# Kernel tuning notes

Measured on AMD Instinct MI355X. Metric: run time of the kernel, lower is better.

## Reference

```python
import jax, jax.numpy as jnp
import numpy as np

N_NODES = 100_000
N_EDGES = 1_000_000
LATENT = 64
HID_ATOM = 256
HID_BOND = 256
RBF_DIM = 32
RBF_DMAX = 10.0
N_ATOM_TYPES = 10
N_CHARGES = 6
N_BOND_ORDERS = 5


def setup_inputs() -> dict:
    key = jax.random.key(0)
    ks = jax.random.split(key, 12)
    positions = jax.random.normal(ks[0], (N_NODES, 3), dtype=jnp.float32) * 5.0
    quantized = jax.random.normal(ks[1], (N_NODES, LATENT), dtype=jnp.float32)
    pair_indices = jax.random.randint(ks[2], (N_EDGES, 2), 0, N_NODES, dtype=jnp.int64)
    s = 0.05
    return {
        "positions": positions,
        "quantized": quantized,
        "pair_indices": pair_indices,
        "aW1": jax.random.normal(ks[3], (LATENT, HID_ATOM), jnp.float32) * s,
        "ab1": jnp.zeros((HID_ATOM,), jnp.float32),
        "aW2": jax.random.normal(ks[4], (HID_ATOM, N_ATOM_TYPES + N_CHARGES), jnp.float32) * s,
        "ab2": jnp.zeros((N_ATOM_TYPES + N_CHARGES,), jnp.float32),
        "bW1": jax.random.normal(ks[5], (LATENT + RBF_DIM, HID_BOND), jnp.float32) * s,
        "bb1": jnp.zeros((HID_BOND,), jnp.float32),
        "bW2": jax.random.normal(ks[6], (HID_BOND, N_BOND_ORDERS), jnp.float32) * s,
        "bb2": jnp.zeros((N_BOND_ORDERS,), jnp.float32),
    }


def _norm_no_nan(x, eps=1e-8):
    # L2 norm over last axis, clamped to avoid NaN gradients at 0
    return jnp.sqrt(jnp.maximum(jnp.sum(x * x, axis=-1), eps))


def _rbf(D, D_min=0.0, D_max=RBF_DMAX, D_count=RBF_DIM):
    mu = jnp.linspace(D_min, D_max, D_count, dtype=D.dtype)  # [D_count]
    sigma = (D_max - D_min) / D_count
    z = (D[..., None] - mu) / sigma
    return jnp.exp(-z * z)  # [E, D_count]


def reference(positions, quantized, pair_indices, aW1, ab1, aW2, ab2, bW1, bb1, bW2, bb2):
    src = pair_indices[:, 0]
    dst = pair_indices[:, 1]
    # pairwise distances -> RBF expansion
    x_i = positions[src]            # [E, 3]
    x_j = positions[dst]
    dists = _rbf(_norm_no_nan(x_i - x_j))  # [E, rbf_dim]
    # atom decoder (per node)
    h = jax.nn.relu(quantized @ aW1 + ab1)
    scalar_logits = h @ aW2 + ab2
    atom_type_logits = scalar_logits[:, :N_ATOM_TYPES]
    atom_charge_logits = scalar_logits[:, N_ATOM_TYPES:]
    # bond decoder (per edge): gathered latent sum concat RBF
    pair_feats = quantized[src] + quantized[dst]           # [E, latent]
    combined = jnp.concatenate([pair_feats, dists], axis=1)  # [E, latent+rbf]
    hb = jax.nn.relu(combined @ bW1 + bb1)
    bond_order_logits = hb @ bW2 + bb2
    return (atom_type_logits, atom_charge_logits, bond_order_logits)
```

## Files before the change

kernel.cpp:

```cpp
#include <hip/hip_runtime.h>
#include <hip/hip_bf16.h>

typedef __bf16 bf16x8 __attribute__((ext_vector_type(8)));
typedef __bf16 bf16x4 __attribute__((ext_vector_type(4)));
typedef float  f32x4  __attribute__((ext_vector_type(4)));

#define N_NODES 100000
#define N_EDGES 1000000
#define LATENT  64
#define HID     256
#define RBF_DIM 32
#define NTYPES  10
#define NCHG    6
#define NBOND   5

#define ATOM_TILES (N_NODES / 32)
#define ANBLK 512

#define ETILE  32
#define ETILES (N_EDGES / ETILE)
#define ENBLK  768

struct __align__(16) ASmem {
    __bf16 qs[32][72];
    __bf16 hsE[32][264];
    float  red[4][2][4][64];
};

template<bool EMIT_QB>
__global__ __launch_bounds__(256, 2) void atom_kernel(
    const float* __restrict__ q,   const float* __restrict__ aW1,
    const float* __restrict__ ab1, const float* __restrict__ aW2,
    const float* __restrict__ ab2, float* __restrict__ outA,
    float* __restrict__ outB,      __bf16* __restrict__ qb)
{
    __shared__ ASmem sm;
    const int t    = threadIdx.x;
    const int w    = t >> 6;
    const int lane = t & 63;
    const int l15  = lane & 15;
    const int hi   = lane >> 4;
    const int wcol = w * 64;

    bf16x8 aw1f[2][4];
    #pragma unroll
    for (int kb = 0; kb < 2; ++kb)
        #pragma unroll
        for (int nt = 0; nt < 4; ++nt) {
            const int nn = wcol + nt * 16 + l15;
            const int k0 = kb * 32 + hi * 8;
            bf16x8 v;
            #pragma unroll
            for (int j = 0; j < 8; ++j) v[j] = (__bf16)aW1[(k0 + j) * HID + nn];
            aw1f[kb][nt] = v;
        }
    bf16x8 aw2f[2];
    #pragma unroll
    for (int kk = 0; kk < 2; ++kk) {
        const int k0 = (w * 2 + kk) * 32 + hi * 8;
        bf16x8 v;
        #pragma unroll
        for (int j = 0; j < 8; ++j) v[j] = (__bf16)aW2[(k0 + j) * 16 + l15];
        aw2f[kk] = v;
    }
    float4 b1v[4];
    #pragma unroll
    for (int nt = 0; nt < 4; ++nt)
        b1v[nt] = *(const float4*)(&ab1[wcol + nt * 16 + hi * 4]);

    const int m_st = t >> 3;
    const int p_st = t & 7;

    for (int tile = blockIdx.x; tile < ATOM_TILES; tile += ANBLK) {
        const int node0 = tile * 32;
        {
            const float* qr = q + (size_t)(node0 + m_st) * 64 + p_st * 8;
            const float4 a0 = *(const float4*)(qr);
            const float4 a1 = *(const float4*)(qr + 4);
            bf16x8 v;
            v[0] = (__bf16)a0.x; v[1] = (__bf16)a0.y; v[2] = (__bf16)a0.z; v[3] = (__bf16)a0.w;
            v[4] = (__bf16)a1.x; v[5] = (__bf16)a1.y; v[6] = (__bf16)a1.z; v[7] = (__bf16)a1.w;
            *(bf16x8*)(&sm.qs[m_st][p_st * 8]) = v;
            if constexpr (EMIT_QB)
                *(bf16x8*)(qb + (size_t)(node0 + m_st) * 64 + p_st * 8) = v;
        }
        __syncthreads();

        f32x4 acc[2][4];
        #pragma unroll
        for (int mt = 0; mt < 2; ++mt)
            #pragma unroll
            for (int nt = 0; nt < 4; ++nt)
                #pragma unroll
                for (int r = 0; r < 4; ++r)
                    acc[mt][nt][r] = ((const float*)&b1v[nt])[r];

        #pragma unroll
        for (int kb = 0; kb < 2; ++kb)
            #pragma unroll
            for (int mt = 0; mt < 2; ++mt) {
                const bf16x8 bq = *(const bf16x8*)((const char*)&sm.qs[0][0]
                                   + (mt * 16 + l15) * 144 + kb * 64 + hi * 16);
                #pragma unroll
                for (int nt = 0; nt < 4; ++nt)
                    acc[mt][nt] = __builtin_amdgcn_mfma_f32_16x16x32_bf16(
                        aw1f[kb][nt], bq, acc[mt][nt], 0, 0, 0);
            }

        #pragma unroll
        for (int mt = 0; mt < 2; ++mt)
            #pragma unroll
            for (int nt = 0; nt < 4; ++nt) {
                bf16x4 hv;
                #pragma unroll
                for (int r = 0; r < 4; ++r)
                    hv[r] = (__bf16)fmaxf(acc[mt][nt][r], 0.f);
                *(bf16x4*)(&sm.hsE[mt * 16 + l15][wcol + nt * 16 + hi * 4]) = hv;
            }
        __syncthreads();

        f32x4 acc2[2];
        {
            f32x4 z = {0.f, 0.f, 0.f, 0.f};
            acc2[0] = z; acc2[1] = z;
        }
        #pragma unroll
        for (int mt = 0; mt < 2; ++mt)
            #pragma unroll
            for (int kk = 0; kk < 2; ++kk) {
                const int kb = w * 2 + kk;
                const bf16x8 af = *(const bf16x8*)((const char*)&sm.hsE[0][0]
                                   + (mt * 16 + l15) * 528 + kb * 64 + hi * 16);
                acc2[mt] = __builtin_amdgcn_mfma_f32_16x16x32_bf16(
                    af, aw2f[kk], acc2[mt], 0, 0, 0);
            }
        #pragma unroll
        for (int mt = 0; mt < 2; ++mt)
            #pragma unroll
            for (int r = 0; r < 4; ++r)
                sm.red[w][mt][r][lane] = acc2[mt][r];
        __syncthreads();

        {
            const int o  = t & 15;
            const int m0 = t >> 4;
            #pragma unroll
            for (int half = 0; half < 2; ++half) {
                const int m  = m0 + half * 16;
                const int mt = m >> 4, rr = m & 15;
                const int hh = rr >> 2, r = rr & 3;
                float s = ab2[o];
                #pragma unroll
                for (int ww = 0; ww < 4; ++ww) s += sm.red[ww][mt][r][hh * 16 + o];
                const int node = node0 + m;
                if (o < NTYPES) outA[node * NTYPES + o] = s;
                else            outB[node * NCHG + (o - NTYPES)] = s;
            }
        }
        __syncthreads();
    }
}

struct __align__(16) ESmem {
    __bf16 comb[2][ETILE][104];
    __bf16 hsE[ETILE][264];
    float  red[2][4][2][4][64];
};

__device__ __forceinline__ void bar_lgkm() {
    asm volatile("s_waitcnt lgkmcnt(0)" ::: "memory");
    __builtin_amdgcn_s_barrier();
}

template<bool USEBF>
__global__ __launch_bounds__(256, 3) void edge_kernel(
    const float* __restrict__ pos, const float* __restrict__ qf,
    const __bf16* __restrict__ qb, const int* __restrict__ pair,
    const float* __restrict__ bW1, const float* __restrict__ bb1,
    const float* __restrict__ bW2, const float* __restrict__ bb2,
    float* __restrict__ outC)
{
    __shared__ ESmem sm;
    const int t    = threadIdx.x;
    const int w    = t >> 6;
    const int lane = t & 63;
    const int l15  = lane & 15;
    const int hi   = lane >> 4;
    const int hid0 = w * 64;

    bf16x8 bw1f[3][4];
    #pragma unroll
    for (int kb = 0; kb < 3; ++kb)
        #pragma unroll
        for (int nt = 0; nt < 4; ++nt) {
            const int nn = hid0 + nt * 16 + l15;
            const int k0 = kb * 32 + hi * 8;
            bf16x8 v;
            #pragma unroll
            for (int j = 0; j < 8; ++j) v[j] = (__bf16)bW1[(k0 + j) * HID + nn];
            bw1f[kb][nt] = v;
        }
    bf16x8 w2f[2];
    #pragma unroll
    for (int kk = 0; kk < 2; ++kk) {
        const int k0 = hid0 + kk * 32 + hi * 8;
        bf16x8 v;
        #pragma unroll
        for (int j = 0; j < 8; ++j)
            v[j] = (l15 < NBOND) ? (__bf16)bW2[(k0 + j) * NBOND + l15] : (__bf16)0.f;
        w2f[kk] = v;
    }
    float4 b1v[4];
    #pragma unroll
    for (int nt = 0; nt < 4; ++nt)
        b1v[nt] = *(const float4*)(&bb1[hid0 + nt * 16 + hi * 4]);

    const int e_loc = t >> 3;
    const int p     = t & 7;

    int tile = blockIdx.x;
    bf16x8 gs, gd;
    float4 fs0, fs1, fd0, fd1;
    float  ps0, ps1, ps2, pd0, pd1, pd2;
    int2 pA = ((const int2*)pair)[(size_t)tile * ETILE + e_loc];
    #define GATHER(pN)                                                            \
        if constexpr (USEBF) {                                                    \
            gs = *(const bf16x8*)(qb + ((unsigned)(pN).x * 64u + (unsigned)(p*8)));\
            gd = *(const bf16x8*)(qb + ((unsigned)(pN).y * 64u + (unsigned)(p*8)));\
        } else {                                                                  \
            fs0 = *(const float4*)(qf + ((unsigned)(pN).x * 64u + (unsigned)(p*8)));     \
            fs1 = *(const float4*)(qf + ((unsigned)(pN).x * 64u + (unsigned)(p*8) + 4u));\
            fd0 = *(const float4*)(qf + ((unsigned)(pN).y * 64u + (unsigned)(p*8)));     \
            fd1 = *(const float4*)(qf + ((unsigned)(pN).y * 64u + (unsigned)(p*8) + 4u));\
        }                                                                         \
        ps0 = pos[(unsigned)(pN).x * 3u];  ps1 = pos[(unsigned)(pN).x * 3u + 1u]; \
        ps2 = pos[(unsigned)(pN).x * 3u + 2u];                                    \
        pd0 = pos[(unsigned)(pN).y * 3u];  pd1 = pos[(unsigned)(pN).y * 3u + 1u]; \
        pd2 = pos[(unsigned)(pN).y * 3u + 2u];

    #define STAGE(buf)                                                            \
        {                                                                         \
            bf16x8 cv;                                                            \
            if constexpr (USEBF) {                                                \
                _Pragma("unroll")                                                 \
                for (int j = 0; j < 8; ++j)                                       \
                    cv[j] = (__bf16)((float)gs[j] + (float)gd[j]);                \
            } else {                                                              \
                cv[0] = (__bf16)(fs0.x + fd0.x); cv[1] = (__bf16)(fs0.y + fd0.y); \
                cv[2] = (__bf16)(fs0.z + fd0.z); cv[3] = (__bf16)(fs0.w + fd0.w); \
                cv[4] = (__bf16)(fs1.x + fd1.x); cv[5] = (__bf16)(fs1.y + fd1.y); \
                cv[6] = (__bf16)(fs1.z + fd1.z); cv[7] = (__bf16)(fs1.w + fd1.w); \
            }                                                                     \
            *(bf16x8*)(&sm.comb[buf][e_loc][p * 8]) = cv;                         \
            const float dx = ps0 - pd0, dy = ps1 - pd1, dz = ps2 - pd2;           \
            const float D  = sqrtf(fmaxf(dx * dx + dy * dy + dz * dz, 1e-8f));    \
            bf16x4 rv;                                                            \
            _Pragma("unroll")                                                     \
            for (int j = 0; j < 4; ++j) {                                         \
                const float mu = (float)(p * 4 + j) * (10.0f / 31.0f);            \
                const float z  = (D - mu) * 3.2f;                                 \
                rv[j] = (__bf16)__expf(-z * z);                                   \
            }                                                                     \
            *(bf16x4*)(&sm.comb[buf][e_loc][64 + p * 4]) = rv;                    \
        }

    GATHER(pA);
    {
        const int tn = tile + ENBLK;
        pA = ((const int2*)pair)[(tn < ETILES ? (size_t)tn * ETILE : 0) + e_loc];
    }
    STAGE(0);
    GATHER(pA);
    {
        const int tn = tile + 2 * ENBLK;
        pA = ((const int2*)pair)[(tn < ETILES ? (size_t)tn * ETILE : 0) + e_loc];
    }
    bar_lgkm();

    int cur = 0;
    int e0_prev = -1;

    for (; tile < ETILES; tile += ENBLK) {
        const int e0 = tile * ETILE;

        if (e0_prev >= 0 && t < 160) {
            const int m = t / 5, o = t % 5;
            const int mt = m >> 4, rr = m & 15;
            const int hh = rr >> 2, r = rr & 3;
            float s = bb2[o];
            #pragma unroll
            for (int ww = 0; ww < 4; ++ww)
                s += sm.red[cur ^ 1][ww][mt][r][hh * 16 + o];
            outC[(size_t)(e0_prev + m) * NBOND + o] = s;
        }

        STAGE(cur ^ 1);

        GATHER(pA);
        {
            const int tn = tile + 3 * ENBLK;
            pA = ((const int2*)pair)[(tn < ETILES ? (size_t)tn * ETILE : 0) + e_loc];
        }

        f32x4 acc[2][4];
        #pragma unroll
        for (int mt = 0; mt < 2; ++mt)
            #pragma unroll
            for (int nt = 0; nt < 4; ++nt)
                #pragma unroll
                for (int r = 0; r < 4; ++r)
                    acc[mt][nt][r] = ((const float*)&b1v[nt])[r];

        #pragma unroll
        for (int kb = 0; kb < 3; ++kb)
            #pragma unroll
            for (int mt = 0; mt < 2; ++mt) {
                const bf16x8 bf = *(const bf16x8*)((const char*)&sm.comb[cur][0][0]
                                   + (mt * 16 + l15) * 208 + kb * 64 + hi * 16);
                #pragma unroll
                for (int nt = 0; nt < 4; ++nt)
                    acc[mt][nt] = __builtin_amdgcn_mfma_f32_16x16x32_bf16(
                        bw1f[kb][nt], bf, acc[mt][nt], 0, 0, 0);
            }
        #pragma unroll
        for (int mt = 0; mt < 2; ++mt)
            #pragma unroll
            for (int nt = 0; nt < 4; ++nt) {
                bf16x4 hv;
                #pragma unroll
                for (int r = 0; r < 4; ++r)
                    hv[r] = (__bf16)fmaxf(acc[mt][nt][r], 0.f);
                *(bf16x4*)((char*)&sm.hsE[0][0]
                           + (mt * 16 + l15) * 528 + (hid0 + nt * 16 + hi * 4) * 2) = hv;
            }

        {
            f32x4 acc2[2];
            {
                f32x4 z = {0.f, 0.f, 0.f, 0.f};
                acc2[0] = z; acc2[1] = z;
            }
            #pragma unroll
            for (int mt = 0; mt < 2; ++mt)
                #pragma unroll
                for (int kk = 0; kk < 2; ++kk) {
                    const bf16x8 af = *(const bf16x8*)((const char*)&sm.hsE[0][0]
                                       + (mt * 16 + l15) * 528
                                       + (hid0 + kk * 32 + hi * 8) * 2);
                    acc2[mt] = __builtin_amdgcn_mfma_f32_16x16x32_bf16(
                        af, w2f[kk], acc2[mt], 0, 0, 0);
                }
            #pragma unroll
            for (int mt = 0; mt < 2; ++mt)
                #pragma unroll
                for (int r = 0; r < 4; ++r)
                    sm.red[cur][w][mt][r][lane] = acc2[mt][r];
        }

        e0_prev = e0;
        bar_lgkm();
        cur ^= 1;
    }

    if (e0_prev >= 0 && t < 160) {
        const int m = t / 5, o = t % 5;
        const int mt = m >> 4, rr = m & 15;
        const int hh = rr >> 2, r = rr & 3;
        float s = bb2[o];
        #pragma unroll
        for (int ww = 0; ww < 4; ++ww)
            s += sm.red[cur ^ 1][ww][mt][r][hh * 16 + o];
        outC[(size_t)(e0_prev + m) * NBOND + o] = s;
    }
    #undef GATHER
    #undef STAGE
}

extern "C" void kernel_launch(void* const* d_in, const int* in_sizes, int n_in,
                              void* d_out, int out_size, void* d_ws, size_t ws_size,
                              hipStream_t stream)
{
    const float* pos = (const float*)d_in[0];
    const float* q   = (const float*)d_in[1];
    const int*   pair= (const int*)  d_in[2];
    const float* aW1 = (const float*)d_in[3];
    const float* ab1 = (const float*)d_in[4];
    const float* aW2 = (const float*)d_in[5];
    const float* ab2 = (const float*)d_in[6];
    const float* bW1 = (const float*)d_in[7];
    const float* bb1 = (const float*)d_in[8];
    const float* bW2 = (const float*)d_in[9];
    const float* bb2 = (const float*)d_in[10];

    float* out  = (float*)d_out;
    float* outA = out;
    float* outB = out + (size_t)N_NODES * NTYPES;
    float* outC = out + (size_t)N_NODES * (NTYPES + NCHG);

    const size_t qb_bytes = (size_t)N_NODES * LATENT * sizeof(__bf16);
    const bool use_bf = (ws_size >= qb_bytes);
    __bf16* qb = (__bf16*)d_ws;

    if (use_bf)
        hipLaunchKernelGGL(atom_kernel<true>, dim3(ANBLK), dim3(256), 0, stream,
                           q, aW1, ab1, aW2, ab2, outA, outB, qb);
    else
        hipLaunchKernelGGL(atom_kernel<false>, dim3(ANBLK), dim3(256), 0, stream,
                           q, aW1, ab1, aW2, ab2, outA, outB, qb);

    if (use_bf)
        hipLaunchKernelGGL(edge_kernel<true>, dim3(ENBLK), dim3(256), 0, stream,
                           pos, q, qb, pair, bW1, bb1, bW2, bb2, outC);
    else
        hipLaunchKernelGGL(edge_kernel<false>, dim3(ENBLK), dim3(256), 0, stream,
                           pos, q, qb, pair, bW1, bb1, bW2, bb2, outC);
}
```

Before: 98.88 us.

## Feed layer-1 MFMA accumulators directly into layer-2 MFMA, drop hidden LDS staging

The edge kernel now applies ReLU to the first-layer MFMA accumulators in registers and passes them straight as A operands to 16x16x16 bf16 MFMAs for the second layer. This removes the per-tile write and read of the hidden activations through shared memory. W2 is re-laid out into four bf16x4 fragments to match the accumulator layout. The smaller shared-memory footprint lets launch bounds rise to 4 blocks per SM and the grid grow to 1024 blocks, at the cost of using twice as many smaller MFMA instructions for the second layer.

```diff
diff --git a/kernel.cpp b/kernel.cpp
--- a/kernel.cpp
+++ b/kernel.cpp
@@ -4,6 +4,7 @@
 typedef __bf16 bf16x8 __attribute__((ext_vector_type(8)));
 typedef __bf16 bf16x4 __attribute__((ext_vector_type(4)));
 typedef float  f32x4  __attribute__((ext_vector_type(4)));
+typedef short  s16x4  __attribute__((ext_vector_type(4)));
 
 #define N_NODES 100000
 #define N_EDGES 1000000
@@ -19,7 +20,21 @@
 
 #define ETILE  32
 #define ETILES (N_EDGES / ETILE)
-#define ENBLK  768
+#define ENBLK  1024
+
+static __device__ __forceinline__ f32x4 mfma16(bf16x4 a, bf16x4 b, f32x4 c) {
+#if __has_builtin(__builtin_amdgcn_mfma_f32_16x16x16bf16_1k)
+    s16x4 ai = __builtin_bit_cast(s16x4, a);
+    s16x4 bi = __builtin_bit_cast(s16x4, b);
+    return __builtin_amdgcn_mfma_f32_16x16x16bf16_1k(ai, bi, c, 0, 0, 0);
+#else
+    asm volatile("s_nop 1\n\t"
+                 "v_mfma_f32_16x16x16_bf16 %0, %1, %2, %0\n\t"
+                 "s_nop 7\n\ts_nop 7"
+                 : "+v"(c) : "v"(a), "v"(b));
+    return c;
+#endif
+}
 
 struct __align__(16) ASmem {
     __bf16 qs[32][72];
@@ -163,7 +178,6 @@
 
 struct __align__(16) ESmem {
     __bf16 comb[2][ETILE][104];
-    __bf16 hsE[ETILE][264];
     float  red[2][4][2][4][64];
 };
 
@@ -173,7 +187,7 @@
 }
 
 template<bool USEBF>
-__global__ __launch_bounds__(256, 3) void edge_kernel(
+__global__ __launch_bounds__(256, 4) void edge_kernel(
     const float* __restrict__ pos, const float* __restrict__ qf,
     const __bf16* __restrict__ qb, const int* __restrict__ pair,
     const float* __restrict__ bW1, const float* __restrict__ bb1,
@@ -200,15 +214,16 @@
             for (int j = 0; j < 8; ++j) v[j] = (__bf16)bW1[(k0 + j) * HID + nn];
             bw1f[kb][nt] = v;
         }
-    bf16x8 w2f[2];
-    #pragma unroll
-    for (int kk = 0; kk < 2; ++kk) {
-        const int k0 = hid0 + kk * 32 + hi * 8;
-        bf16x8 v;
-        #pragma unroll
-        for (int j = 0; j < 8; ++j)
-            v[j] = (l15 < NBOND) ? (__bf16)bW2[(k0 + j) * NBOND + l15] : (__bf16)0.f;
-        w2f[kk] = v;
+    bf16x4 w2f[4];
+    #pragma unroll
+    for (int nt = 0; nt < 4; ++nt) {
+        bf16x4 v;
+        #pragma unroll
+        for (int j = 0; j < 4; ++j)
+            v[j] = (l15 < NBOND)
+                 ? (__bf16)bW2[(hid0 + nt * 16 + hi * 4 + j) * NBOND + l15]
+                 : (__bf16)0.f;
+        w2f[nt] = v;
     }
     float4 b1v[4];
     #pragma unroll
@@ -322,17 +337,6 @@
                     acc[mt][nt] = __builtin_amdgcn_mfma_f32_16x16x32_bf16(
                         bw1f[kb][nt], bf, acc[mt][nt], 0, 0, 0);
             }
-        #pragma unroll
-        for (int mt = 0; mt < 2; ++mt)
-            #pragma unroll
-            for (int nt = 0; nt < 4; ++nt) {
-                bf16x4 hv;
-                #pragma unroll
-                for (int r = 0; r < 4; ++r)
-                    hv[r] = (__bf16)fmaxf(acc[mt][nt][r], 0.f);
-                *(bf16x4*)((char*)&sm.hsE[0][0]
-                           + (mt * 16 + l15) * 528 + (hid0 + nt * 16 + hi * 4) * 2) = hv;
-            }
 
         {
             f32x4 acc2[2];
@@ -343,12 +347,12 @@
             #pragma unroll
             for (int mt = 0; mt < 2; ++mt)
                 #pragma unroll
-                for (int kk = 0; kk < 2; ++kk) {
-                    const bf16x8 af = *(const bf16x8*)((const char*)&sm.hsE[0][0]
-                                       + (mt * 16 + l15) * 528
-                                       + (hid0 + kk * 32 + hi * 8) * 2);
-                    acc2[mt] = __builtin_amdgcn_mfma_f32_16x16x32_bf16(
-                        af, w2f[kk], acc2[mt], 0, 0, 0);
+                for (int nt = 0; nt < 4; ++nt) {
+                    bf16x4 hv;
+                    #pragma unroll
+                    for (int r = 0; r < 4; ++r)
+                        hv[r] = (__bf16)fmaxf(acc[mt][nt][r], 0.f);
+                    acc2[mt] = mfma16(hv, w2f[nt], acc2[mt]);
                 }
             #pragma unroll
             for (int mt = 0; mt < 2; ++mt)
```

New measurement: 142.1 us. 43.7% more time.
